# Kernel optimization log

Hardware: AMD Instinct MI355X
Metric: run time of the kernel (lower is better)

Reference implementation:

```python
import jax, jax.numpy as jnp
import numpy as np

GRID_SIZE = 5
SPLINE_ORDER = 3
GRID_RANGE = (-1.0, 1.0)


def b_splines(x, grid, spline_order=SPLINE_ORDER):
    # x: [B, in], grid: [G] with G = grid_size + 2*spline_order + 1
    x = x[..., None]                      # [B, in, 1]
    g = grid[None, None, :]               # [1, 1, G]
    bases = ((x >= g[..., :-1]) & (x < g[..., 1:])).astype(x.dtype)  # [B, in, G-1]
    for k in range(1, spline_order + 1):
        left = (x - g[..., :-(k + 1)]) / (g[..., k:-1] - g[..., :-(k + 1)]) * bases[..., :-1]
        right = (g[..., k + 1:] - x) / (g[..., k + 1:] - g[..., 1:-k]) * bases[..., 1:]
        bases = left + right
    return bases                          # [B, in, grid_size + spline_order]


def setup_inputs() -> dict:
    key = jax.random.key(0)
    k1, k2, k3, k4 = jax.random.split(key, 4)
    B, IN, OUT = 32768, 256, 256
    n_coef = GRID_SIZE + SPLINE_ORDER  # 8
    h = (GRID_RANGE[1] - GRID_RANGE[0]) / GRID_SIZE
    grid = jnp.arange(-SPLINE_ORDER, GRID_SIZE + SPLINE_ORDER + 1, dtype=jnp.float32) * h + GRID_RANGE[0]  # [12]
    x = jax.random.normal(k1, (B, IN), dtype=jnp.float32)
    base_weight = jax.random.normal(k2, (OUT, IN), dtype=jnp.float32) * np.sqrt(2.0 / IN)
    spline_weight = jax.random.normal(k3, (OUT, IN, n_coef), dtype=jnp.float32) * (0.1 / GRID_SIZE)
    spline_scaler = jax.random.normal(k4, (OUT, IN), dtype=jnp.float32) * np.sqrt(2.0 / IN)
    return {"x": x, "base_weight": base_weight, "spline_weight": spline_weight,
            "spline_scaler": spline_scaler, "grid": grid}


def reference(x, base_weight, spline_weight, spline_scaler, grid):
    B = x.shape[0]
    out_features = base_weight.shape[0]
    # base branch: silu(x) @ base_weight^T
    base_out = jnp.matmul(jax.nn.silu(x), base_weight.T)  # [B, out]
    # spline branch
    bases = b_splines(x, grid)                             # [B, in, n_coef]
    scaled_w = spline_weight * spline_scaler[..., None]    # [out, in, n_coef]
    spline_out = jnp.matmul(bases.reshape(B, -1), scaled_w.reshape(out_features, -1).T)
    return base_out + spline_out
```

## Files before the change

kernel.cpp:

```cpp
#include <hip/hip_runtime.h>
#include <hip/hip_bf16.h>
#include <stdint.h>


#define IN_F 256
#define OUT_F 256
#define KDIM 2304
#define BK 64
#define NCHUNK (KDIM / BK)
#define WC_BYTES ((size_t)OUT_F * KDIM * 2)

#define AS1 __attribute__((address_space(1)))
#define AS3 __attribute__((address_space(3)))

typedef float f32x4 __attribute__((ext_vector_type(4)));
typedef short bf16x8 __attribute__((ext_vector_type(8)));

__device__ __forceinline__ uint32_t f2bf(float f) {
    union { float f; uint32_t u; } c; c.f = f;
    uint32_t u = c.u;
    return (u + 0x7FFFu + ((u >> 16) & 1u)) >> 16;
}

__device__ __forceinline__ float silu_f(float v) {
    return v / (1.0f + __expf(-v));
}

__global__ void build_w(const float* __restrict__ bw, const float* __restrict__ sw,
                        const float* __restrict__ ss, unsigned short* __restrict__ Wc) {
    const int o = blockIdx.x;
    const int i = threadIdx.x;
    Wc[o * KDIM + i] = (unsigned short)f2bf(bw[o * IN_F + i]);
    const float scal = ss[o * IN_F + i];
    const float4* swv = reinterpret_cast<const float4*>(sw + (size_t)(o * IN_F + i) * 8);
    float4 s0 = swv[0], s1 = swv[1];
    uint4 wv;
    wv.x = f2bf(s0.x * scal) | (f2bf(s0.y * scal) << 16);
    wv.y = f2bf(s0.z * scal) | (f2bf(s0.w * scal) << 16);
    wv.z = f2bf(s1.x * scal) | (f2bf(s1.y * scal) << 16);
    wv.w = f2bf(s1.z * scal) | (f2bf(s1.w * scal) << 16);
    *reinterpret_cast<uint4*>(Wc + o * KDIM + IN_F + i * 8) = wv;
}

__launch_bounds__(512, 4)
__global__ void kan_fused(const float* __restrict__ x, const unsigned short* __restrict__ Wc,
                          float* __restrict__ out) {
    __shared__ __align__(16) unsigned short As[2][128 * 64];
    __shared__ __align__(16) unsigned short Bs[2][128 * 64];

    const int bid = blockIdx.x;
    const int row0 = (bid >> 1) * 128;
    const int col0 = (bid & 1) * 128;
    const int tid = threadIdx.x;
    const int lane = tid & 63;
    const int w = tid >> 6;
    const int wm = w >> 2;
    const int wn = w & 3;
    const int l15 = lane & 15;
    const int q = lane >> 4;

    const int sr = lane >> 3;
    const int s  = lane & 7;
    const int g  = s ^ sr;
    const int srow = w * 16 + sr;

    const char* wb0 = (const char*)(Wc + (size_t)(col0 + srow) * KDIM + g * 8);
    const char* wb1 = (const char*)(Wc + (size_t)(col0 + srow + 8) * KDIM + g * 8);
    const int ldst0 = (w * 16) * 64;
    const int ldst1 = (w * 16 + 8) * 64;

    const float* xs0 = x + (size_t)(row0 + srow) * IN_F + g * 8;
    const float* xs1 = xs0 + 8 * IN_F;
    const float* xb0 = x + (size_t)(row0 + srow) * IN_F + g;
    const float* xb1 = xb0 + 8 * IN_F;

    int aoffh[2][4], boffh[2][2];
#pragma unroll
    for (int ks = 0; ks < 2; ++ks) {
        const int g0 = ks * 4 + q;
#pragma unroll
        for (int mt = 0; mt < 4; ++mt) {
            int r = wm * 64 + mt * 16 + l15;
            aoffh[ks][mt] = r * 64 + ((g0 ^ (r & 7)) << 3);
        }
#pragma unroll
        for (int nt = 0; nt < 2; ++nt) {
            int r = wn * 32 + nt * 16 + l15;
            boffh[ks][nt] = r * 64 + ((g0 ^ (r & 7)) << 3);
        }
    }

    f32x4 acc[4][2] = {};
    float xr[2][8];
    uint64_t pk2[2];
    int j02[2];

    auto stage_b = [&](int kc, int buf) {
        __builtin_amdgcn_global_load_lds((const AS1 void*)(wb0 + kc * 128),
                                         (AS3 void*)&Bs[buf][ldst0], 16, 0, 0);
        __builtin_amdgcn_global_load_lds((const AS1 void*)(wb1 + kc * 128),
                                         (AS3 void*)&Bs[buf][ldst1], 16, 0, 0);
    };
    auto load_x = [&](int kc) {
        if (kc < 4) {
            const float* p0 = xs0 + kc * 64;
            const float* p1 = xs1 + kc * 64;
            float4 a0 = *reinterpret_cast<const float4*>(p0);
            float4 b0 = *reinterpret_cast<const float4*>(p0 + 4);
            float4 a1 = *reinterpret_cast<const float4*>(p1);
            float4 b1 = *reinterpret_cast<const float4*>(p1 + 4);
            xr[0][0] = a0.x; xr[0][1] = a0.y; xr[0][2] = a0.z; xr[0][3] = a0.w;
            xr[0][4] = b0.x; xr[0][5] = b0.y; xr[0][6] = b0.z; xr[0][7] = b0.w;
            xr[1][0] = a1.x; xr[1][1] = a1.y; xr[1][2] = a1.z; xr[1][3] = a1.w;
            xr[1][4] = b1.x; xr[1][5] = b1.y; xr[1][6] = b1.z; xr[1][7] = b1.w;
        } else {
            float xx0 = *xb0;
            float xx1 = *xb1;
            xb0 += 8; xb1 += 8;
#pragma unroll
            for (int j = 0; j < 2; ++j) {
                float xx = j ? xx1 : xx0;
                float u = __builtin_fmaf(xx, 2.5f, 5.5f);
                float jf = floorf(u);
                float t = u - jf;
                j02[j] = (int)jf;
                float t2 = t * t, t3 = t2 * t;
                float p3 = t3 * (1.0f / 6.0f);
                float p2 = -0.5f * t3 + 0.5f * t2 + 0.5f * t + (1.0f / 6.0f);
                float p1 = 0.5f * t3 - t2 + (2.0f / 3.0f);
                float omt = 1.0f - t;
                float p0 = omt * omt * omt * (1.0f / 6.0f);
                pk2[j] = (uint64_t)f2bf(p0) | ((uint64_t)f2bf(p1) << 16) |
                         ((uint64_t)f2bf(p2) << 32) | ((uint64_t)f2bf(p3) << 48);
            }
        }
    };
    auto write_a = [&](int kc, int buf) {
        if (kc < 4) {
#pragma unroll
            for (int j = 0; j < 2; ++j) {
                uint4 wv;
                wv.x = f2bf(silu_f(xr[j][0])) | (f2bf(silu_f(xr[j][1])) << 16);
                wv.y = f2bf(silu_f(xr[j][2])) | (f2bf(silu_f(xr[j][3])) << 16);
                wv.z = f2bf(silu_f(xr[j][4])) | (f2bf(silu_f(xr[j][5])) << 16);
                wv.w = f2bf(silu_f(xr[j][6])) | (f2bf(silu_f(xr[j][7])) << 16);
                *reinterpret_cast<uint4*>(&As[buf][(srow + j * 8) * 64 + s * 8]) = wv;
            }
        } else {
#pragma unroll
            for (int j = 0; j < 2; ++j) {
                int j0 = j02[j];
                uint64_t pk = ((unsigned)j0 <= 10u) ? pk2[j] : 0ull;
                int jc = j0 < 0 ? 0 : (j0 > 10 ? 10 : j0);
                int sh = jc * 16 - 48;
                unsigned __int128 v = (unsigned __int128)pk;
                v = (sh >= 0) ? (v << sh) : (v >> (-sh));
                uint4 wv;
                wv.x = (uint32_t)v;
                wv.y = (uint32_t)(v >> 32);
                wv.z = (uint32_t)(v >> 64);
                wv.w = (uint32_t)(v >> 96);
                *reinterpret_cast<uint4*>(&As[buf][(srow + j * 8) * 64 + s * 8]) = wv;
            }
        }
    };

    stage_b(0, 0);
    load_x(0);
    write_a(0, 0);
    __syncthreads();

    for (int kc = 0; kc < NCHUNK; ++kc) {
        const int cur = kc & 1;
        const int nxt = cur ^ 1;
        if (kc + 1 < NCHUNK) {
            stage_b(kc + 1, nxt);
            load_x(kc + 1);
        }
#pragma unroll
        for (int ks = 0; ks < 2; ++ks) {
            bf16x8 af[4], bfv[2];
#pragma unroll
            for (int mt = 0; mt < 4; ++mt)
                af[mt] = *reinterpret_cast<const bf16x8*>(&As[cur][aoffh[ks][mt]]);
#pragma unroll
            for (int nt = 0; nt < 2; ++nt)
                bfv[nt] = *reinterpret_cast<const bf16x8*>(&Bs[cur][boffh[ks][nt]]);
#pragma unroll
            for (int mt = 0; mt < 4; ++mt)
#pragma unroll
                for (int nt = 0; nt < 2; ++nt)
                    acc[mt][nt] = __builtin_amdgcn_mfma_f32_16x16x32_bf16(
                        af[mt], bfv[nt], acc[mt][nt], 0, 0, 0);
        }
        if (kc + 1 < NCHUNK) write_a(kc + 1, nxt);
        __syncthreads();
    }

    float* outp = out + (size_t)(row0 + wm * 64 + q * 4) * OUT_F + col0 + wn * 32 + l15;
#pragma unroll
    for (int mt = 0; mt < 4; ++mt) {
#pragma unroll
        for (int nt = 0; nt < 2; ++nt) {
#pragma unroll
            for (int r = 0; r < 4; ++r)
                outp[(size_t)(mt * 16 + r) * OUT_F + nt * 16] = acc[mt][nt][r];
        }
    }
}

extern "C" void kernel_launch(void* const* d_in, const int* in_sizes, int n_in,
                              void* d_out, int out_size, void* d_ws, size_t ws_size,
                              hipStream_t stream) {
    const float* x  = (const float*)d_in[0];
    const float* bw = (const float*)d_in[1];
    const float* sw = (const float*)d_in[2];
    const float* ss = (const float*)d_in[3];
    unsigned short* Wc = (unsigned short*)d_ws;

    build_w<<<dim3(OUT_F), dim3(IN_F), 0, stream>>>(bw, sw, ss, Wc);

    const int B_ROWS = in_sizes[0] / IN_F;
    kan_fused<<<dim3(B_ROWS / 128 * 2), dim3(512), 0, stream>>>(x, Wc, (float*)d_out);
}
```

Baseline: 152.8 us.

## Widen block tile to full 256 output columns to avoid recomputing A

Each block now covers 128 rows by all 256 output columns instead of 128 columns, so the silu and B-spline A tile is built once per row block rather than twice. Each wave holds a 64x64 accumulator tile (16 MFMA accumulators), and the B staging buffer doubles to 256x64. The main loop is manually unrolled by two with fixed ping-pong buffers. The costs are more registers and LDS per block (launch bounds lowered to 2 blocks per CU) and half as many blocks in the grid.

After: 150.2 us. No clear change (-1.7%).

```diff
diff --git a/kernel.cpp b/kernel.cpp
--- a/kernel.cpp
+++ b/kernel.cpp
@@ -42,15 +42,15 @@
     *reinterpret_cast<uint4*>(Wc + o * KDIM + IN_F + i * 8) = wv;
 }
 
-__launch_bounds__(512, 4)
+__launch_bounds__(512, 2)
 __global__ void kan_fused(const float* __restrict__ x, const unsigned short* __restrict__ Wc,
                           float* __restrict__ out) {
-    __shared__ __align__(16) unsigned short As[2][128 * 64];
-    __shared__ __align__(16) unsigned short Bs[2][128 * 64];
-
-    const int bid = blockIdx.x;
-    const int row0 = (bid >> 1) * 128;
-    const int col0 = (bid & 1) * 128;
+    __shared__ __align__(16) unsigned short As0[128 * 64];
+    __shared__ __align__(16) unsigned short As1[128 * 64];
+    __shared__ __align__(16) unsigned short Bs0[256 * 64];
+    __shared__ __align__(16) unsigned short Bs1[256 * 64];
+
+    const int row0 = blockIdx.x * 128;
     const int tid = threadIdx.x;
     const int lane = tid & 63;
     const int w = tid >> 6;
@@ -64,42 +64,25 @@
     const int g  = s ^ sr;
     const int srow = w * 16 + sr;
 
-    const char* wb0 = (const char*)(Wc + (size_t)(col0 + srow) * KDIM + g * 8);
-    const char* wb1 = (const char*)(Wc + (size_t)(col0 + srow + 8) * KDIM + g * 8);
-    const int ldst0 = (w * 16) * 64;
-    const int ldst1 = (w * 16 + 8) * 64;
+    const int brow = w * 32 + sr;
 
     const float* xs0 = x + (size_t)(row0 + srow) * IN_F + g * 8;
     const float* xs1 = xs0 + 8 * IN_F;
-    const float* xb0 = x + (size_t)(row0 + srow) * IN_F + g;
-    const float* xb1 = xb0 + 8 * IN_F;
-
-    int aoffh[2][4], boffh[2][2];
-#pragma unroll
-    for (int ks = 0; ks < 2; ++ks) {
-        const int g0 = ks * 4 + q;
-#pragma unroll
-        for (int mt = 0; mt < 4; ++mt) {
-            int r = wm * 64 + mt * 16 + l15;
-            aoffh[ks][mt] = r * 64 + ((g0 ^ (r & 7)) << 3);
-        }
-#pragma unroll
-        for (int nt = 0; nt < 2; ++nt) {
-            int r = wn * 32 + nt * 16 + l15;
-            boffh[ks][nt] = r * 64 + ((g0 ^ (r & 7)) << 3);
-        }
-    }
-
-    f32x4 acc[4][2] = {};
+
+    f32x4 acc[4][4] = {};
     float xr[2][8];
     uint64_t pk2[2];
     int j02[2];
 
-    auto stage_b = [&](int kc, int buf) {
-        __builtin_amdgcn_global_load_lds((const AS1 void*)(wb0 + kc * 128),
-                                         (AS3 void*)&Bs[buf][ldst0], 16, 0, 0);
-        __builtin_amdgcn_global_load_lds((const AS1 void*)(wb1 + kc * 128),
-                                         (AS3 void*)&Bs[buf][ldst1], 16, 0, 0);
+    auto stage_b = [&](int kc, unsigned short* Bsb) {
+#pragma unroll
+        for (int j = 0; j < 4; ++j) {
+            const unsigned short* gp =
+                Wc + (size_t)(brow + j * 8) * KDIM + kc * BK + g * 8;
+            __builtin_amdgcn_global_load_lds((const AS1 void*)gp,
+                                             (AS3 void*)&Bsb[(w * 32 + j * 8) * 64],
+                                             16, 0, 0);
+        }
     };
     auto load_x = [&](int kc) {
         if (kc < 4) {
@@ -114,9 +97,9 @@
             xr[1][0] = a1.x; xr[1][1] = a1.y; xr[1][2] = a1.z; xr[1][3] = a1.w;
             xr[1][4] = b1.x; xr[1][5] = b1.y; xr[1][6] = b1.z; xr[1][7] = b1.w;
         } else {
-            float xx0 = *xb0;
-            float xx1 = *xb1;
-            xb0 += 8; xb1 += 8;
+            const int i0 = (kc - 4) * 8 + g;
+            float xx0 = xs0[i0 - g * 8];
+            float xx1 = xs1[i0 - g * 8];
 #pragma unroll
             for (int j = 0; j < 2; ++j) {
                 float xx = j ? xx1 : xx0;
@@ -135,7 +118,7 @@
             }
         }
     };
-    auto write_a = [&](int kc, int buf) {
+    auto write_a = [&](int kc, unsigned short* Asb) {
         if (kc < 4) {
 #pragma unroll
             for (int j = 0; j < 2; ++j) {
@@ -144,7 +127,7 @@
                 wv.y = f2bf(silu_f(xr[j][2])) | (f2bf(silu_f(xr[j][3])) << 16);
                 wv.z = f2bf(silu_f(xr[j][4])) | (f2bf(silu_f(xr[j][5])) << 16);
                 wv.w = f2bf(silu_f(xr[j][6])) | (f2bf(silu_f(xr[j][7])) << 16);
-                *reinterpret_cast<uint4*>(&As[buf][(srow + j * 8) * 64 + s * 8]) = wv;
+                *reinterpret_cast<uint4*>(&Asb[(srow + j * 8) * 64 + s * 8]) = wv;
             }
         } else {
 #pragma unroll
@@ -160,48 +143,64 @@
                 wv.y = (uint32_t)(v >> 32);
                 wv.z = (uint32_t)(v >> 64);
                 wv.w = (uint32_t)(v >> 96);
-                *reinterpret_cast<uint4*>(&As[buf][(srow + j * 8) * 64 + s * 8]) = wv;
-            }
-        }
-    };
-
-    stage_b(0, 0);
-    load_x(0);
-    write_a(0, 0);
-    __syncthreads();
-
-    for (int kc = 0; kc < NCHUNK; ++kc) {
-        const int cur = kc & 1;
-        const int nxt = cur ^ 1;
-        if (kc + 1 < NCHUNK) {
-            stage_b(kc + 1, nxt);
-            load_x(kc + 1);
-        }
+                *reinterpret_cast<uint4*>(&Asb[(srow + j * 8) * 64 + s * 8]) = wv;
+            }
+        }
+    };
+    auto mfma_chunk = [&](const unsigned short* Asb, const unsigned short* Bsb) {
 #pragma unroll
         for (int ks = 0; ks < 2; ++ks) {
-            bf16x8 af[4], bfv[2];
+            const int g0 = ks * 4 + q;
+            bf16x8 af[4], bfv[4];
+#pragma unroll
+            for (int mt = 0; mt < 4; ++mt) {
+                int r = wm * 64 + mt * 16 + l15;
+                af[mt] = *reinterpret_cast<const bf16x8*>(
+                    &Asb[r * 64 + ((g0 ^ (r & 7)) << 3)]);
+            }
+#pragma unroll
+            for (int nt = 0; nt < 4; ++nt) {
+                int r = wn * 64 + nt * 16 + l15;
+                bfv[nt] = *reinterpret_cast<const bf16x8*>(
+                    &Bsb[r * 64 + ((g0 ^ (r & 7)) << 3)]);
+            }
 #pragma unroll
             for (int mt = 0; mt < 4; ++mt)
-                af[mt] = *reinterpret_cast<const bf16x8*>(&As[cur][aoffh[ks][mt]]);
-#pragma unroll
-            for (int nt = 0; nt < 2; ++nt)
-                bfv[nt] = *reinterpret_cast<const bf16x8*>(&Bs[cur][boffh[ks][nt]]);
-#pragma unroll
-            for (int mt = 0; mt < 4; ++mt)
-#pragma unroll
-                for (int nt = 0; nt < 2; ++nt)
+#pragma unroll
+                for (int nt = 0; nt < 4; ++nt)
                     acc[mt][nt] = __builtin_amdgcn_mfma_f32_16x16x32_bf16(
                         af[mt], bfv[nt], acc[mt][nt], 0, 0, 0);
         }
-        if (kc + 1 < NCHUNK) write_a(kc + 1, nxt);
-        __syncthreads();
+    };
+
+#define CHUNK_STEP(KC, ASC, BSC, ASN, BSN)            \
+    {                                                 \
+        if ((KC) + 1 < NCHUNK) {                      \
+            stage_b((KC) + 1, BSN);                   \
+            load_x((KC) + 1);                         \
+        }                                             \
+        mfma_chunk(ASC, BSC);                         \
+        if ((KC) + 1 < NCHUNK) write_a((KC) + 1, ASN);\
+        __syncthreads();                              \
     }
 
-    float* outp = out + (size_t)(row0 + wm * 64 + q * 4) * OUT_F + col0 + wn * 32 + l15;
+    stage_b(0, Bs0);
+    load_x(0);
+    write_a(0, As0);
+    __syncthreads();
+
+#pragma unroll 1
+    for (int it = 0; it < NCHUNK / 2; ++it) {
+        const int kc0 = it * 2;
+        CHUNK_STEP(kc0,     As0, Bs0, As1, Bs1)
+        CHUNK_STEP(kc0 + 1, As1, Bs1, As0, Bs0)
+    }
+
+    float* outp = out + (size_t)(row0 + wm * 64 + q * 4) * OUT_F + wn * 64 + l15;
 #pragma unroll
     for (int mt = 0; mt < 4; ++mt) {
 #pragma unroll
-        for (int nt = 0; nt < 2; ++nt) {
+        for (int nt = 0; nt < 4; ++nt) {
 #pragma unroll
             for (int r = 0; r < 4; ++r)
                 outp[(size_t)(mt * 16 + r) * OUT_F + nt * 16] = acc[mt][nt][r];
@@ -221,5 +220,5 @@
     build_w<<<dim3(OUT_F), dim3(IN_F), 0, stream>>>(bw, sw, ss, Wc);
 
     const int B_ROWS = in_sizes[0] / IN_F;
-    kan_fused<<<dim3(B_ROWS / 128 * 2), dim3(512), 0, stream>>>(x, Wc, (float*)d_out);
-}
+    kan_fused<<<dim3(B_ROWS / 128), dim3(512), 0, stream>>>(x, Wc, (float*)d_out);
+}
```
